# Optimization experiments

Measured on AMD Instinct MI355X. Metric: run time of the kernel, lower is better.

## Reference

```python
import jax, jax.numpy as jnp
import numpy as np

DIM = 1024
NUM_HEADS = 16
HEAD_DIM = DIM // NUM_HEADS
SCALE = HEAD_DIM ** -0.5


def setup_inputs() -> dict:
    key = jax.random.key(0)
    k1, k2, k3 = jax.random.split(key, 3)
    B, N = 2, 2048
    x = jax.random.normal(k1, (B, N, DIM), dtype=jnp.float32)
    W_qkv = jax.random.normal(k2, (DIM, 3 * DIM), dtype=jnp.float32) * (DIM ** -0.5)
    b_qkv = jnp.zeros((3 * DIM,), dtype=jnp.float32)
    W_proj = jax.random.normal(k3, (DIM, DIM), dtype=jnp.float32) * (DIM ** -0.5)
    b_proj = jnp.zeros((DIM,), dtype=jnp.float32)
    return {"x": x, "W_qkv": W_qkv, "b_qkv": b_qkv, "W_proj": W_proj, "b_proj": b_proj}


def reference(x, W_qkv, b_qkv, W_proj, b_proj):
    B, N, D = x.shape
    qkv = x @ W_qkv + b_qkv                      # [B, N, 3D]
    qkv = qkv.reshape(B, N, 3, NUM_HEADS, HEAD_DIM)
    qkv = jnp.transpose(qkv, (2, 0, 3, 1, 4))    # [3, B, H, N, hd]
    q, k, v = qkv[0], qkv[1], qkv[2]
    attn = jnp.einsum('bhqd,bhkd->bhqk', q, k) * SCALE  # [B, H, N, N]
    attn = jax.nn.softmax(attn, axis=-1)
    out = jnp.einsum('bhqk,bhkd->bhqd', attn, v)        # [B, H, N, hd]
    out = jnp.transpose(out, (0, 2, 1, 3)).reshape(B, N, D)
    out = out @ W_proj + b_proj
    return out
```

## Files before the change

kernel.cpp:

```cpp
#include <hip/hip_runtime.h>


typedef __bf16 bf16_t;
typedef __bf16 bf16x2 __attribute__((ext_vector_type(2)));
typedef __bf16 bf16x4 __attribute__((ext_vector_type(4)));
typedef __bf16 bf16x8 __attribute__((ext_vector_type(8)));
typedef float  f32x4  __attribute__((ext_vector_type(4)));

#define NTOK 2048
#define DIM  1024
#define NH   16
#define HD   64
#define SCL2 0.18033688011112042f

#define MFMA16(a, b, c) __builtin_amdgcn_mfma_f32_16x16x32_bf16((a), (b), (c), 0, 0, 0)

__device__ __forceinline__ void gload_lds16(const void* g, void* l) {
  __builtin_amdgcn_global_load_lds((const __attribute__((address_space(1))) void*)g,
                                   (__attribute__((address_space(3))) void*)l, 16, 0, 0);
}

__device__ __forceinline__ void transpose_cvt_tile(const float* __restrict__ W,
                                                   bf16_t* __restrict__ WT,
                                                   int rows, int cols, int bx, int by) {
  __shared__ float tile[32][33];
  int j0 = bx * 32, i0 = by * 32;
  int c = threadIdx.x & 31, r0 = threadIdx.x >> 5;
#pragma unroll
  for (int it = 0; it < 4; ++it) {
    int r = r0 + it * 8;
    tile[r][c] = W[(long)(i0 + r) * cols + j0 + c];
  }
  __syncthreads();
#pragma unroll
  for (int it = 0; it < 4; ++it) {
    int r = r0 + it * 8;
    WT[(long)(j0 + r) * rows + i0 + c] = (bf16_t)tile[c][r];
  }
}

__global__ __launch_bounds__(256) void k_prep(const float* __restrict__ x,
                                              bf16_t* __restrict__ xb,
                                              const float* __restrict__ Wq,
                                              bf16_t* __restrict__ WqT,
                                              const float* __restrict__ Wp,
                                              bf16_t* __restrict__ WpT) {
  int id = blockIdx.x;
  if (id < 2048) {
    int i = (id * 256 + threadIdx.x) * 8;
    float4 a = *(const float4*)(x + i);
    float4 b = *(const float4*)(x + i + 4);
    bf16x8 v;
    v[0] = (bf16_t)a.x; v[1] = (bf16_t)a.y; v[2] = (bf16_t)a.z; v[3] = (bf16_t)a.w;
    v[4] = (bf16_t)b.x; v[5] = (bf16_t)b.y; v[6] = (bf16_t)b.z; v[7] = (bf16_t)b.w;
    *(bf16x8*)(xb + i) = v;
  } else if (id < 2048 + 3072) {
    int t = id - 2048;
    transpose_cvt_tile(Wq, WqT, 1024, 3072, t % 96, t / 96);
  } else {
    int t = id - 5120;
    transpose_cvt_tile(Wp, WpT, 1024, 1024, t & 31, t >> 5);
  }
}

__device__ __forceinline__ void gemm_core(const bf16_t* __restrict__ A,
                                          const bf16_t* __restrict__ B,
                                          int K, int bm, int bn,
                                          bf16_t* As, bf16_t* Bs, f32x4 acc[4][4]) {
  const int t = threadIdx.x;
  const int lane = t & 63;
  const int w = t >> 6;
  const int wr = (w >> 1) * 64, wc = (w & 1) * 64;
  const int l15 = lane & 15, g = lane >> 4;
  const int srow = t >> 2, scol = (t & 3) * 8;
  const f32x4 vzero = {0.f, 0.f, 0.f, 0.f};
#pragma unroll
  for (int m = 0; m < 4; ++m)
#pragma unroll
    for (int n = 0; n < 4; ++n) acc[m][n] = vzero;

  const bf16_t* ga = A + (long)(bm + srow) * K + scol;
  const bf16_t* gb = B + (long)(bn + srow) * K + scol;
  bf16_t* lA = As + srow * 32 + scol;
  bf16_t* lB = Bs + srow * 32 + scol;
  const long rstep = 64l * K;

  for (int k0 = 0; k0 < K; k0 += 32) {
    gload_lds16(ga + k0,         lA);
    gload_lds16(ga + rstep + k0, lA + 64 * 32);
    gload_lds16(gb + k0,         lB);
    gload_lds16(gb + rstep + k0, lB + 64 * 32);
    __syncthreads();
    bf16x8 af[4], bfv[4];
#pragma unroll
    for (int m = 0; m < 4; ++m)
      af[m] = *(const bf16x8*)(As + (wr + m * 16 + l15) * 32 + g * 8);
#pragma unroll
    for (int n = 0; n < 4; ++n)
      bfv[n] = *(const bf16x8*)(Bs + (wc + n * 16 + l15) * 32 + g * 8);
#pragma unroll
    for (int m = 0; m < 4; ++m)
#pragma unroll
      for (int n = 0; n < 4; ++n)
        acc[m][n] = MFMA16(af[m], bfv[n], acc[m][n]);
    __syncthreads();
  }
}

__global__ __launch_bounds__(256) void k_gemm_qkv(const bf16_t* __restrict__ xb,
                                                  const bf16_t* __restrict__ WqT,
                                                  const float* __restrict__ bq,
                                                  bf16_t* __restrict__ Qb,
                                                  bf16_t* __restrict__ Kb,
                                                  bf16_t* __restrict__ Vt) {
  __shared__ alignas(16) bf16_t As[128 * 32];
  __shared__ alignas(16) bf16_t Bs[128 * 32];
  f32x4 acc[4][4];
  const int bm = blockIdx.y * 128, bn = blockIdx.x * 128;
  gemm_core(xb, WqT, DIM, bm, bn, As, Bs, acc);

  const int lane = threadIdx.x & 63, w = threadIdx.x >> 6;
  const int wr = (w >> 1) * 64, wc = (w & 1) * 64;
  const int l15 = lane & 15, g = lane >> 4;
#pragma unroll
  for (int n = 0; n < 4; ++n) {
    int col = bn + wc + n * 16 + l15;
    float bias = bq[col];
    int t3 = col >> 10, rem = col & 1023;
    int h = rem >> 6, d = rem & 63;
#pragma unroll
    for (int m = 0; m < 4; ++m) {
      int rowb = bm + wr + m * 16 + g * 4;
#pragma unroll
      for (int r = 0; r < 4; ++r) {
        int row = rowb + r;
        int b = row >> 11, tok = row & 2047;
        int bh = b * NH + h;
        float val = acc[m][n][r] + bias;
        if (t3 == 0) {
          Qb[bh * (NTOK * HD) + tok * HD + d] = (bf16_t)(val * SCL2);
        } else if (t3 == 1) {
          int rr = tok & 63;
          int off = bh * (NTOK * HD) + (tok >> 6) * 4096 + rr * 64 +
                    (((d >> 3) ^ (rr & 7)) << 3) + (d & 7);
          Kb[off] = (bf16_t)val;
        } else {
          int ct = tok & 63;
          int off = bh * (NTOK * HD) + (tok >> 6) * 4096 + d * 64 +
                    (((ct >> 3) ^ (d & 7)) << 3) + (ct & 7);
          Vt[off] = (bf16_t)val;
        }
      }
    }
  }
}

__global__ __launch_bounds__(256, 4) void k_attn(const bf16_t* __restrict__ Qb,
                                                 const bf16_t* __restrict__ Kb,
                                                 const bf16_t* __restrict__ Vt,
                                                 bf16_t* __restrict__ Ob) {
  __shared__ alignas(16) bf16_t Ks[2][64 * 64];
  __shared__ alignas(16) bf16_t Vs[2][64 * 64];
  __shared__ alignas(16) char  P2[4][2048];

  const int b0 = blockIdx.x;
  const int swz = (b0 & 7) * 128 + (b0 >> 3);
  const int qt = swz & 31, bh = swz >> 5;
  const int b = bh >> 4, h = bh & 15;
  const int t = threadIdx.x;
  const int w = t >> 6, lane = t & 63;
  const int l15 = lane & 15, g = lane >> 4;
  const bf16_t* Qp = Qb + bh * (NTOK * HD);
  const bf16_t* Kp = Kb + bh * (NTOK * HD);
  const bf16_t* Vp = Vt + bh * (NTOK * HD);
  const int q0 = qt * 64 + w * 16;
  char* P2w = &P2[w][0];

  const int cs0 = ((g ^ (l15 & 7)) << 4);
  const int cs1 = cs0 ^ 64;

  bf16x8 qfr[2];
#pragma unroll
  for (int kk = 0; kk < 2; ++kk)
    qfr[kk] = *(const bf16x8*)(Qp + (q0 + l15) * HD + kk * 32 + g * 8);

  bf16x8 ones;
#pragma unroll
  for (int i = 0; i < 8; ++i) ones[i] = (bf16_t)1.0f;

  const f32x4 vzero = {0.f, 0.f, 0.f, 0.f};
  f32x4 o[4];
#pragma unroll
  for (int df = 0; df < 4; ++df) o[df] = vzero;
  f32x4 o_sum = vzero;

  auto stage = [&](int buf, int tile) {
    const bf16_t* gk = Kp + tile * 4096 + t * 8;
    const bf16_t* gv = Vp + tile * 4096 + t * 8;
    gload_lds16(gk,        (char*)Ks[buf] + t * 16);
    gload_lds16(gk + 2048, (char*)Ks[buf] + 4096 + t * 16);
    gload_lds16(gv,        (char*)Vs[buf] + t * 16);
    gload_lds16(gv + 2048, (char*)Vs[buf] + 4096 + t * 16);
  };

  stage(0, 0);
  __syncthreads();
  int cur = 0;

  for (int kt = 0; kt < NTOK; kt += 64) {
    if (kt + 64 < NTOK) stage(cur ^ 1, (kt >> 6) + 1);
    const char* kbuf = (const char*)Ks[cur];
    const char* vbuf = (const char*)Vs[cur];
    f32x4 s[4];
    __builtin_amdgcn_s_setprio(1);
#pragma unroll
    for (int kf = 0; kf < 4; ++kf) {
      int rb = (kf * 16 + l15) * 128;
      bf16x8 ka0 = *(const bf16x8*)(kbuf + rb + cs0);
      bf16x8 ka1 = *(const bf16x8*)(kbuf + rb + cs1);
      s[kf] = MFMA16(ka0, qfr[0], vzero);
      s[kf] = MFMA16(ka1, qfr[1], s[kf]);
    }
    __builtin_amdgcn_s_setprio(0);
#pragma unroll
    for (int kf = 0; kf < 4; ++kf) {
      bf16x4 pw;
      pw[0] = (bf16_t)__builtin_amdgcn_exp2f(s[kf][0]);
      pw[1] = (bf16_t)__builtin_amdgcn_exp2f(s[kf][1]);
      pw[2] = (bf16_t)__builtin_amdgcn_exp2f(s[kf][2]);
      pw[3] = (bf16_t)__builtin_amdgcn_exp2f(s[kf][3]);
      *(bf16x4*)(P2w + (2 * kf + (g >> 1)) * 256 + l15 * 16 + 8 * (g & 1)) = pw;
    }
    __builtin_amdgcn_s_setprio(1);
#pragma unroll
    for (int kb = 0; kb < 2; ++kb) {
      bf16x8 pf = *(const bf16x8*)(P2w + kb * 1024 + lane * 16);
      int csk = kb ? cs1 : cs0;
      o_sum = MFMA16(ones, pf, o_sum);
#pragma unroll
      for (int df = 0; df < 4; ++df) {
        bf16x8 va = *(const bf16x8*)(vbuf + (df * 16 + l15) * 128 + csk);
        o[df] = MFMA16(va, pf, o[df]);
      }
    }
    __builtin_amdgcn_s_setprio(0);
    __syncthreads();
    cur ^= 1;
  }
  float inv = 1.0f / o_sum[0];
  int tok = q0 + l15;
  bf16_t* op = Ob + (long)(b * NTOK + tok) * DIM + h * HD;
#pragma unroll
  for (int df = 0; df < 4; ++df) {
#pragma unroll
    for (int rp = 0; rp < 2; ++rp) {
      bf16x2 v2;
      v2[0] = (bf16_t)(o[df][rp * 2]     * inv);
      v2[1] = (bf16_t)(o[df][rp * 2 + 1] * inv);
      *(bf16x2*)(op + df * 16 + g * 4 + rp * 2) = v2;
    }
  }
}

__global__ __launch_bounds__(256) void k_gemm_proj(const bf16_t* __restrict__ Ob,
                                                   const bf16_t* __restrict__ WpT,
                                                   const float* __restrict__ bp,
                                                   float* __restrict__ out) {
  __shared__ alignas(16) bf16_t As[128 * 32];
  __shared__ alignas(16) bf16_t Bs[128 * 32];
  f32x4 acc[4][4];
  const int bm = blockIdx.y * 128, bn = blockIdx.x * 128;
  gemm_core(Ob, WpT, DIM, bm, bn, As, Bs, acc);

  const int lane = threadIdx.x & 63, w = threadIdx.x >> 6;
  const int wr = (w >> 1) * 64, wc = (w & 1) * 64;
  const int l15 = lane & 15, g = lane >> 4;
#pragma unroll
  for (int n = 0; n < 4; ++n) {
    int col = bn + wc + n * 16 + l15;
    float bias = bp[col];
#pragma unroll
    for (int m = 0; m < 4; ++m) {
      int rowb = bm + wr + m * 16 + g * 4;
#pragma unroll
      for (int r = 0; r < 4; ++r)
        out[(long)(rowb + r) * DIM + col] = acc[m][n][r] + bias;
    }
  }
}

extern "C" void kernel_launch(void* const* d_in, const int* in_sizes, int n_in,
                              void* d_out, int out_size, void* d_ws, size_t ws_size,
                              hipStream_t stream) {
  const float* x     = (const float*)d_in[0];
  const float* Wqkv  = (const float*)d_in[1];
  const float* bqkv  = (const float*)d_in[2];
  const float* Wproj = (const float*)d_in[3];
  const float* bproj = (const float*)d_in[4];
  float* out = (float*)d_out;

  char* ws = (char*)d_ws;
  bf16_t* xb  = (bf16_t*)(ws);
  bf16_t* WqT = (bf16_t*)(ws + (8l  << 20));
  bf16_t* WpT = (bf16_t*)(ws + (14l << 20));
  bf16_t* Qb  = (bf16_t*)(ws + (16l << 20));
  bf16_t* Kb  = (bf16_t*)(ws + (24l << 20));
  bf16_t* Vt  = (bf16_t*)(ws + (32l << 20));
  bf16_t* Ob  = (bf16_t*)(ws);

  k_prep<<<6144, 256, 0, stream>>>(x, xb, Wqkv, WqT, Wproj, WpT);
  k_gemm_qkv<<<dim3(24, 32), 256, 0, stream>>>(xb, WqT, bqkv, Qb, Kb, Vt);
  k_attn<<<1024, 256, 0, stream>>>(Qb, Kb, Vt, Ob);
  k_gemm_proj<<<dim3(8, 32), 256, 0, stream>>>(Ob, WpT, bproj, out);
}
```

Measured before the change: 125.7 us.

## Process two query fragments per wave in attention to reuse K/V tiles

Each attention wave now handles 32 query rows (two 16-row fragments) instead of 16, so each block covers 128 queries and the grid is halved to 512 blocks. Every K and V fragment read from LDS feeds two MFMAs, which halves the K/V global and LDS traffic per query. The cost is more accumulator registers (launch bounds drop to 3 blocks per CU), a larger P buffer in shared memory, and fewer blocks to spread across the CUs.

```diff
diff --git a/kernel.cpp b/kernel.cpp
--- a/kernel.cpp
+++ b/kernel.cpp
@@ -155,17 +155,17 @@
   }
 }
 
-__global__ __launch_bounds__(256, 4) void k_attn(const bf16_t* __restrict__ Qb,
+__global__ __launch_bounds__(256, 3) void k_attn(const bf16_t* __restrict__ Qb,
                                                  const bf16_t* __restrict__ Kb,
                                                  const bf16_t* __restrict__ Vt,
                                                  bf16_t* __restrict__ Ob) {
   __shared__ alignas(16) bf16_t Ks[2][64 * 64];
   __shared__ alignas(16) bf16_t Vs[2][64 * 64];
-  __shared__ alignas(16) char  P2[4][2048];
+  __shared__ alignas(16) char  P2[4][4096];
 
   const int b0 = blockIdx.x;
-  const int swz = (b0 & 7) * 128 + (b0 >> 3);
-  const int qt = swz & 31, bh = swz >> 5;
+  const int swz = (b0 & 7) * 64 + (b0 >> 3);
+  const int qt = swz & 15, bh = swz >> 4;
   const int b = bh >> 4, h = bh & 15;
   const int t = threadIdx.x;
   const int w = t >> 6, lane = t & 63;
@@ -173,26 +173,30 @@
   const bf16_t* Qp = Qb + bh * (NTOK * HD);
   const bf16_t* Kp = Kb + bh * (NTOK * HD);
   const bf16_t* Vp = Vt + bh * (NTOK * HD);
-  const int q0 = qt * 64 + w * 16;
+  const int q0 = qt * 128 + w * 32;
   char* P2w = &P2[w][0];
 
   const int cs0 = ((g ^ (l15 & 7)) << 4);
   const int cs1 = cs0 ^ 64;
 
-  bf16x8 qfr[2];
-#pragma unroll
-  for (int kk = 0; kk < 2; ++kk)
-    qfr[kk] = *(const bf16x8*)(Qp + (q0 + l15) * HD + kk * 32 + g * 8);
+  bf16x8 qfr[2][2];
+#pragma unroll
+  for (int qf = 0; qf < 2; ++qf)
+#pragma unroll
+    for (int kk = 0; kk < 2; ++kk)
+      qfr[qf][kk] = *(const bf16x8*)(Qp + (q0 + qf * 16 + l15) * HD + kk * 32 + g * 8);
 
   bf16x8 ones;
 #pragma unroll
   for (int i = 0; i < 8; ++i) ones[i] = (bf16_t)1.0f;
 
   const f32x4 vzero = {0.f, 0.f, 0.f, 0.f};
-  f32x4 o[4];
-#pragma unroll
-  for (int df = 0; df < 4; ++df) o[df] = vzero;
-  f32x4 o_sum = vzero;
+  f32x4 o[2][4];
+#pragma unroll
+  for (int qf = 0; qf < 2; ++qf)
+#pragma unroll
+    for (int df = 0; df < 4; ++df) o[qf][df] = vzero;
+  f32x4 o_sum[2] = {vzero, vzero};
 
   auto stage = [&](int buf, int tile) {
     const bf16_t* gk = Kp + tile * 4096 + t * 8;
@@ -211,53 +215,63 @@
     if (kt + 64 < NTOK) stage(cur ^ 1, (kt >> 6) + 1);
     const char* kbuf = (const char*)Ks[cur];
     const char* vbuf = (const char*)Vs[cur];
-    f32x4 s[4];
+    f32x4 s[2][4];
     __builtin_amdgcn_s_setprio(1);
 #pragma unroll
     for (int kf = 0; kf < 4; ++kf) {
       int rb = (kf * 16 + l15) * 128;
       bf16x8 ka0 = *(const bf16x8*)(kbuf + rb + cs0);
       bf16x8 ka1 = *(const bf16x8*)(kbuf + rb + cs1);
-      s[kf] = MFMA16(ka0, qfr[0], vzero);
-      s[kf] = MFMA16(ka1, qfr[1], s[kf]);
+      s[0][kf] = MFMA16(ka0, qfr[0][0], vzero);
+      s[1][kf] = MFMA16(ka0, qfr[1][0], vzero);
+      s[0][kf] = MFMA16(ka1, qfr[0][1], s[0][kf]);
+      s[1][kf] = MFMA16(ka1, qfr[1][1], s[1][kf]);
     }
     __builtin_amdgcn_s_setprio(0);
 #pragma unroll
-    for (int kf = 0; kf < 4; ++kf) {
-      bf16x4 pw;
-      pw[0] = (bf16_t)__builtin_amdgcn_exp2f(s[kf][0]);
-      pw[1] = (bf16_t)__builtin_amdgcn_exp2f(s[kf][1]);
-      pw[2] = (bf16_t)__builtin_amdgcn_exp2f(s[kf][2]);
-      pw[3] = (bf16_t)__builtin_amdgcn_exp2f(s[kf][3]);
-      *(bf16x4*)(P2w + (2 * kf + (g >> 1)) * 256 + l15 * 16 + 8 * (g & 1)) = pw;
-    }
+    for (int qf = 0; qf < 2; ++qf)
+#pragma unroll
+      for (int kf = 0; kf < 4; ++kf) {
+        bf16x4 pw;
+        pw[0] = (bf16_t)__builtin_amdgcn_exp2f(s[qf][kf][0]);
+        pw[1] = (bf16_t)__builtin_amdgcn_exp2f(s[qf][kf][1]);
+        pw[2] = (bf16_t)__builtin_amdgcn_exp2f(s[qf][kf][2]);
+        pw[3] = (bf16_t)__builtin_amdgcn_exp2f(s[qf][kf][3]);
+        *(bf16x4*)(P2w + qf * 2048 + (2 * kf + (g >> 1)) * 256 + l15 * 16 + 8 * (g & 1)) = pw;
+      }
     __builtin_amdgcn_s_setprio(1);
 #pragma unroll
     for (int kb = 0; kb < 2; ++kb) {
-      bf16x8 pf = *(const bf16x8*)(P2w + kb * 1024 + lane * 16);
+      bf16x8 pf0 = *(const bf16x8*)(P2w + kb * 1024 + lane * 16);
+      bf16x8 pf1 = *(const bf16x8*)(P2w + 2048 + kb * 1024 + lane * 16);
       int csk = kb ? cs1 : cs0;
-      o_sum = MFMA16(ones, pf, o_sum);
+      o_sum[0] = MFMA16(ones, pf0, o_sum[0]);
+      o_sum[1] = MFMA16(ones, pf1, o_sum[1]);
 #pragma unroll
       for (int df = 0; df < 4; ++df) {
         bf16x8 va = *(const bf16x8*)(vbuf + (df * 16 + l15) * 128 + csk);
-        o[df] = MFMA16(va, pf, o[df]);
+        o[0][df] = MFMA16(va, pf0, o[0][df]);
+        o[1][df] = MFMA16(va, pf1, o[1][df]);
       }
     }
     __builtin_amdgcn_s_setprio(0);
     __syncthreads();
     cur ^= 1;
   }
-  float inv = 1.0f / o_sum[0];
-  int tok = q0 + l15;
-  bf16_t* op = Ob + (long)(b * NTOK + tok) * DIM + h * HD;
-#pragma unroll
-  for (int df = 0; df < 4; ++df) {
-#pragma unroll
-    for (int rp = 0; rp < 2; ++rp) {
-      bf16x2 v2;
-      v2[0] = (bf16_t)(o[df][rp * 2]     * inv);
-      v2[1] = (bf16_t)(o[df][rp * 2 + 1] * inv);
-      *(bf16x2*)(op + df * 16 + g * 4 + rp * 2) = v2;
+#pragma unroll
+  for (int qf = 0; qf < 2; ++qf) {
+    float inv = 1.0f / o_sum[qf][0];
+    int tok = q0 + qf * 16 + l15;
+    bf16_t* op = Ob + (long)(b * NTOK + tok) * DIM + h * HD;
+#pragma unroll
+    for (int df = 0; df < 4; ++df) {
+#pragma unroll
+      for (int rp = 0; rp < 2; ++rp) {
+        bf16x2 v2;
+        v2[0] = (bf16_t)(o[qf][df][rp * 2]     * inv);
+        v2[1] = (bf16_t)(o[qf][df][rp * 2 + 1] * inv);
+        *(bf16x2*)(op + df * 16 + g * 4 + rp * 2) = v2;
+      }
     }
   }
 }
@@ -310,6 +324,6 @@
 
   k_prep<<<6144, 256, 0, stream>>>(x, xb, Wqkv, WqT, Wproj, WpT);
   k_gemm_qkv<<<dim3(24, 32), 256, 0, stream>>>(xb, WqT, bqkv, Qb, Kb, Vt);
-  k_attn<<<1024, 256, 0, stream>>>(Qb, Kb, Vt, Ob);
+  k_attn<<<512, 256, 0, stream>>>(Qb, Kb, Vt, Ob);
   k_gemm_proj<<<dim3(8, 32), 256, 0, stream>>>(Ob, WpT, bproj, out);
 }
```

Result: faster. 120.0 us (-4.5%).
